# Kernel tuning notes

Measured on AMD Instinct MI355X. Metric: run time of the kernel, lower is better.

## Reference

```python
import jax, jax.numpy as jnp
import numpy as np

NEG_SLOPE = 0.2
EPS = 1e-16


def _gat_conv(x, src, dst, edge_attr, W, We, att_src, att_dst, att_edge, bias):
    """PyG GATConv, heads=H, concat=False, edge_dim given. x:[N,F_in]."""
    N = x.shape[0]
    H, C = att_src.shape
    xs = (x @ W.T).reshape(N, H, C)                      # [N,H,C]
    a_src = jnp.einsum('nhc,hc->nh', xs, att_src)        # [N,H]
    a_dst = jnp.einsum('nhc,hc->nh', xs, att_dst)        # [N,H]
    e = (edge_attr @ We.T).reshape(-1, H, C)             # [E,H,C]
    a_edge = jnp.einsum('ehc,hc->eh', e, att_edge)       # [E,H]
    alpha = a_src[src] + a_dst[dst] + a_edge             # [E,H]
    alpha = jax.nn.leaky_relu(alpha, NEG_SLOPE)
    # segment softmax over destination nodes (per head)
    amax = jax.ops.segment_max(alpha, dst, num_segments=N)   # [N,H]
    ex = jnp.exp(alpha - amax[dst])
    denom = jax.ops.segment_sum(ex, dst, num_segments=N)     # [N,H]
    alpha = ex / (denom[dst] + EPS)
    msg = xs[src] * alpha[..., None]                     # [E,H,C]
    out = jax.ops.segment_sum(msg, dst, num_segments=N)  # [N,H,C]
    return out.mean(axis=1) + bias                       # concat=False -> mean over heads


def _add_self_loops(src, dst, edge_attr, N):
    # PyG add_self_loops with fill_value='mean': per-dst mean of incoming edge_attr
    ones = jnp.ones((edge_attr.shape[0],), edge_attr.dtype)
    sums = jax.ops.segment_sum(edge_attr, dst, num_segments=N)
    cnt = jax.ops.segment_sum(ones, dst, num_segments=N)
    loop_attr = sums / jnp.maximum(cnt, 1.0)[:, None]
    idx = jnp.arange(N, dtype=src.dtype)
    return (jnp.concatenate([src, idx]), jnp.concatenate([dst, idx]),
            jnp.concatenate([edge_attr, loop_attr], axis=0))


def setup_inputs() -> dict:
    key = jax.random.key(0)
    ks = jax.random.split(key, 16)
    N, E, F_IN, C, H = 100000, 1600000, 64, 32, 4
    s = 0.1
    inp = {
        'x': jax.random.normal(ks[0], (N, F_IN), jnp.float32),
        'edge_index': jax.random.randint(ks[1], (2, E), 0, N, jnp.int32),
        'edge_weight': jax.random.uniform(ks[2], (E, 1), jnp.float32),
        'w1': jax.random.normal(ks[3], (H * C, F_IN), jnp.float32) * s,
        'we1': jax.random.normal(ks[4], (H * C, 1), jnp.float32) * s,
        'as1': jax.random.normal(ks[5], (H, C), jnp.float32) * s,
        'ad1': jax.random.normal(ks[6], (H, C), jnp.float32) * s,
        'ae1': jax.random.normal(ks[7], (H, C), jnp.float32) * s,
        'b1': jnp.zeros((C,), jnp.float32),
        'w2': jax.random.normal(ks[8], (H * C, C), jnp.float32) * s,
        'we2': jax.random.normal(ks[9], (H * C, 1), jnp.float32) * s,
        'as2': jax.random.normal(ks[10], (H, C), jnp.float32) * s,
        'ad2': jax.random.normal(ks[11], (H, C), jnp.float32) * s,
        'ae2': jax.random.normal(ks[12], (H, C), jnp.float32) * s,
        'b2': jnp.zeros((C,), jnp.float32),
    }
    return inp


def reference(x, edge_index, edge_weight, w1, we1, as1, ad1, ae1, b1,
              w2, we2, as2, ad2, ae2, b2):
    N = x.shape[0]
    src, dst, ea = _add_self_loops(edge_index[0], edge_index[1], edge_weight, N)
    h = jax.nn.relu(_gat_conv(x, src, dst, ea, w1, we1, as1, ad1, ae1, b1))
    # nn.Dropout is identity in eval mode
    h = jax.nn.relu(_gat_conv(h, src, dst, ea, w2, we2, as2, ad2, ae2, b2))
    return h
```

## Files before the change

### kernel.cpp

```cpp
#include <hip/hip_runtime.h>
#include <hip/hip_fp16.h>
#include <cstddef>

#define GAT_EPS 1e-16f
#define CAP 48

__global__ __launch_bounds__(256, 2)
void k_gemm1h(const float* __restrict__ x, const float* __restrict__ W,
              const float* __restrict__ as_, const float* __restrict__ ad_,
              __half* __restrict__ xs, float* __restrict__ asrc,
              float* __restrict__ adst, int N, int gemmb,
              const int* __restrict__ src, const int* __restrict__ dst,
              const float* __restrict__ ew, int* __restrict__ cnt,
              int2* __restrict__ epk, int E,
              const float* __restrict__ we1, const float* __restrict__ ae1,
              const float* __restrict__ we2, const float* __restrict__ ae2,
              float* __restrict__ wd,
              const float* __restrict__ as2, const float* __restrict__ ad2,
              const float* __restrict__ W2, float* __restrict__ vs2,
              float* __restrict__ vd2) {
    if (blockIdx.x == gridDim.x - 1) {
        int t = threadIdx.x;
        if (t < 128) {
            float v1 = we1[t] * ae1[t];
            float v2 = we2[t] * ae2[t];
#pragma unroll
            for (int off = 16; off; off >>= 1) {
                v1 += __shfl_xor(v1, off);
                v2 += __shfl_xor(v2, off);
            }
            if ((t & 31) == 0) { wd[t >> 5] = v1; wd[4 + (t >> 5)] = v2; }
            int h = t >> 5, c = t & 31;
            float s = 0.f, dv = 0.f;
            for (int k = 0; k < 32; k++) {
                float w = W2[(h * 32 + k) * 32 + c];
                s  += as2[h * 32 + k] * w;
                dv += ad2[h * 32 + k] * w;
            }
            vs2[t] = s;
            vd2[t] = dv;
        }
        return;
    }
    int g = blockIdx.x / 5;
    int r = blockIdx.x % 5;
    if (r != 0) {
        int i = (g * 4 + r - 1) * 256 + threadIdx.x;
        if (i < E) {
            int d = dst[i];
            int p = atomicAdd(&cnt[d], 1);
            p = min(p, CAP - 1);
            int2 q; q.x = src[i]; q.y = __float_as_int(ew[i]);
            epk[(size_t)d * CAP + p] = q;
        }
        return;
    }
    if (g >= gemmb) return;

    int n0 = g * 64;
    int t = threadIdx.x;
    int tx = t & 31;
    int ty = t >> 5;
    __shared__ __half Wh[64 * 132];
    __shared__ float xsh[64 * 65];
    int nrows = min(64, N - n0);
    for (int j = t; j < 8192; j += 256) {
        int c = j >> 6, k = j & 63;
        Wh[k * 132 + ((c & 31) << 2) + (c >> 5)] = __float2half(W[j]);
    }
    const float* xg = x + (size_t)n0 * 64;
    for (int j = t; j < nrows * 64; j += 256) xsh[(j >> 6) * 65 + (j & 63)] = xg[j];
    __syncthreads();

    float acc[8][4];
#pragma unroll
    for (int i = 0; i < 8; i++)
#pragma unroll
        for (int j = 0; j < 4; j++) acc[i][j] = 0.f;

#pragma unroll 4
    for (int k = 0; k < 64; k++) {
        const __half2* wp = reinterpret_cast<const __half2*>(&Wh[k * 132 + (tx << 2)]);
        float2 wf0 = __half22float2(wp[0]);
        float2 wf1 = __half22float2(wp[1]);
#pragma unroll
        for (int i = 0; i < 8; i++) {
            float xv = xsh[(ty * 8 + i) * 65 + k];
            acc[i][0] += xv * wf0.x;
            acc[i][1] += xv * wf0.y;
            acc[i][2] += xv * wf1.x;
            acc[i][3] += xv * wf1.y;
        }
    }

    float asv[4], adv[4];
#pragma unroll
    for (int j = 0; j < 4; j++) { asv[j] = as_[32 * j + tx]; adv[j] = ad_[32 * j + tx]; }

#pragma unroll
    for (int i = 0; i < 8; i++) {
        int row = ty * 8 + i;
        bool ok = row < nrows;
        __half* orow = xs + (size_t)(n0 + row) * 128;
#pragma unroll
        for (int j = 0; j < 4; j++) {
            if (ok) orow[32 * j + tx] = __float2half(acc[i][j]);
            float vs = acc[i][j] * asv[j];
            float vd = acc[i][j] * adv[j];
#pragma unroll
            for (int off = 16; off; off >>= 1) {
                vs += __shfl_xor(vs, off);
                vd += __shfl_xor(vd, off);
            }
            if (ok && tx == 0) {
                asrc[(size_t)(n0 + row) * 4 + j] = vs;
                adst[(size_t)(n0 + row) * 4 + j] = vd;
            }
        }
    }
}

__global__ void k_gather1(const int2* __restrict__ epk, const int* __restrict__ cnt,
                          const __half* __restrict__ xs,
                          const float* __restrict__ asrc, const float* __restrict__ adst,
                          const float* __restrict__ wedot, const float* __restrict__ bias,
                          const float* __restrict__ vs2, const float* __restrict__ vd2,
                          __half2* __restrict__ h1, float* __restrict__ asrc2,
                          float* __restrict__ adst2, int N) {
    int node = blockIdx.x * 4 + (threadIdx.x >> 6);
    if (node >= N) return;
    int l = threadIdx.x & 63;
    int q = l >> 4;
    int p = l & 15;
    int h = p >> 2;
    float wd = wedot[h];
    float ad = adst[(size_t)node * 4 + h];
    int cv = min(cnt[node], CAP);
    int beg = node * CAP;
    int end = beg + cv;

    float a0 = 0.f, a1 = 0.f, a2 = 0.f, a3 = 0.f;
    float a4 = 0.f, a5 = 0.f, a6 = 0.f, a7 = 0.f, ds = 0.f, easum = 0.f;
#pragma unroll 2
    for (int i = beg; i < end; i += 4) {
        int idx = i + q;
        bool valid = idx < end;
        int2 e = epk[valid ? idx : end - 1];
        int s = e.x;
        float eav = valid ? __int_as_float(e.y) : 0.f;
        easum += eav;
        float as = asrc[(size_t)s * 4 + h];
        float al = as + ad + __int_as_float(e.y) * wd;
        al = fmaxf(al, 0.2f * al);
        float w = valid ? __expf(al) : 0.f;
        uint4 raw = reinterpret_cast<const uint4*>(xs + (size_t)s * 128)[p];
        const __half2* hp = reinterpret_cast<const __half2*>(&raw);
        float2 f0 = __half22float2(hp[0]);
        float2 f1 = __half22float2(hp[1]);
        float2 f2 = __half22float2(hp[2]);
        float2 f3 = __half22float2(hp[3]);
        a0 += w * f0.x; a1 += w * f0.y;
        a2 += w * f1.x; a3 += w * f1.y;
        a4 += w * f2.x; a5 += w * f2.y;
        a6 += w * f3.x; a7 += w * f3.y;
        ds += w;
    }
    easum += __shfl_xor(easum, 16);
    easum += __shfl_xor(easum, 32);
    float loop_ea = easum / fmaxf((float)cv, 1.0f);
    float aln = asrc[(size_t)node * 4 + h] + ad + loop_ea * wd;
    aln = fmaxf(aln, 0.2f * aln);
    float wl = __expf(aln);
    if (q == 0) {
        uint4 raw = reinterpret_cast<const uint4*>(xs + (size_t)node * 128)[p];
        const __half2* hp = reinterpret_cast<const __half2*>(&raw);
        float2 f0 = __half22float2(hp[0]);
        float2 f1 = __half22float2(hp[1]);
        float2 f2 = __half22float2(hp[2]);
        float2 f3 = __half22float2(hp[3]);
        a0 += wl * f0.x; a1 += wl * f0.y;
        a2 += wl * f1.x; a3 += wl * f1.y;
        a4 += wl * f2.x; a5 += wl * f2.y;
        a6 += wl * f3.x; a7 += wl * f3.y;
        ds += wl;
    }
    a0 += __shfl_xor(a0, 16); a1 += __shfl_xor(a1, 16);
    a2 += __shfl_xor(a2, 16); a3 += __shfl_xor(a3, 16);
    a4 += __shfl_xor(a4, 16); a5 += __shfl_xor(a5, 16);
    a6 += __shfl_xor(a6, 16); a7 += __shfl_xor(a7, 16);
    ds += __shfl_xor(ds, 16);
    a0 += __shfl_xor(a0, 32); a1 += __shfl_xor(a1, 32);
    a2 += __shfl_xor(a2, 32); a3 += __shfl_xor(a3, 32);
    a4 += __shfl_xor(a4, 32); a5 += __shfl_xor(a5, 32);
    a6 += __shfl_xor(a6, 32); a7 += __shfl_xor(a7, 32);
    ds += __shfl_xor(ds, 32);
    float inv = 1.f / (ds + GAT_EPS);
    a0 *= inv; a1 *= inv; a2 *= inv; a3 *= inv;
    a4 *= inv; a5 *= inv; a6 *= inv; a7 *= inv;
    a0 += __shfl_xor(a0, 4); a1 += __shfl_xor(a1, 4);
    a2 += __shfl_xor(a2, 4); a3 += __shfl_xor(a3, 4);
    a4 += __shfl_xor(a4, 4); a5 += __shfl_xor(a5, 4);
    a6 += __shfl_xor(a6, 4); a7 += __shfl_xor(a7, 4);
    a0 += __shfl_xor(a0, 8); a1 += __shfl_xor(a1, 8);
    a2 += __shfl_xor(a2, 8); a3 += __shfl_xor(a3, 8);
    a4 += __shfl_xor(a4, 8); a5 += __shfl_xor(a5, 8);
    a6 += __shfl_xor(a6, 8); a7 += __shfl_xor(a7, 8);
    if (l < 4) {
        int c0 = l * 8;
        float rv[8];
        rv[0] = fmaxf(0.25f * a0 + bias[c0 + 0], 0.f);
        rv[1] = fmaxf(0.25f * a1 + bias[c0 + 1], 0.f);
        rv[2] = fmaxf(0.25f * a2 + bias[c0 + 2], 0.f);
        rv[3] = fmaxf(0.25f * a3 + bias[c0 + 3], 0.f);
        rv[4] = fmaxf(0.25f * a4 + bias[c0 + 4], 0.f);
        rv[5] = fmaxf(0.25f * a5 + bias[c0 + 5], 0.f);
        rv[6] = fmaxf(0.25f * a6 + bias[c0 + 6], 0.f);
        rv[7] = fmaxf(0.25f * a7 + bias[c0 + 7], 0.f);
        __half2* hp = h1 + (size_t)node * 16 + l * 4;
        hp[0] = __floats2half2_rn(rv[0], rv[1]);
        hp[1] = __floats2half2_rn(rv[2], rv[3]);
        hp[2] = __floats2half2_rn(rv[4], rv[5]);
        hp[3] = __floats2half2_rn(rv[6], rv[7]);
        float pa[4] = {0.f, 0.f, 0.f, 0.f}, pd[4] = {0.f, 0.f, 0.f, 0.f};
#pragma unroll
        for (int hh = 0; hh < 4; hh++)
#pragma unroll
            for (int j = 0; j < 8; j++) {
                pa[hh] += rv[j] * vs2[hh * 32 + c0 + j];
                pd[hh] += rv[j] * vd2[hh * 32 + c0 + j];
            }
#pragma unroll
        for (int hh = 0; hh < 4; hh++) {
            pa[hh] += __shfl_xor(pa[hh], 1);
            pa[hh] += __shfl_xor(pa[hh], 2);
            pd[hh] += __shfl_xor(pd[hh], 1);
            pd[hh] += __shfl_xor(pd[hh], 2);
        }
        if (l == 0) {
            float4 wa, wb;
            wa.x = pa[0]; wa.y = pa[1]; wa.z = pa[2]; wa.w = pa[3];
            wb.x = pd[0]; wb.y = pd[1]; wb.z = pd[2]; wb.w = pd[3];
            *reinterpret_cast<float4*>(asrc2 + (size_t)node * 4) = wa;
            *reinterpret_cast<float4*>(adst2 + (size_t)node * 4) = wb;
        }
    }
}

__global__ void k_gather2(const int2* __restrict__ epk, const int* __restrict__ cnt,
                          const __half2* __restrict__ h1,
                          const float* __restrict__ asrc, const float* __restrict__ adst,
                          const float* __restrict__ wedot, const float* __restrict__ W2,
                          const float* __restrict__ bias, float* __restrict__ out, int N) {
    __shared__ unsigned int Wsh[2180];
    int t = threadIdx.x;
    for (int j = t; j < 2048; j += 256) {
        int rr = j >> 4, kk = j & 15;
        __half2 hv = __floats2half2_rn(W2[rr * 32 + 2 * kk], W2[rr * 32 + 2 * kk + 1]);
        Wsh[rr * 17 + (rr >> 5) + kk] = *reinterpret_cast<unsigned int*>(&hv);
    }
    __syncthreads();
    int node = blockIdx.x * 4 + (t >> 6);
    if (node >= N) return;
    int l = t & 63;
    int q = l >> 4;
    int p = l & 15;
    int h = l & 3;
    int base = l & 48;
    float wd = wedot[h];
    float ad = adst[(size_t)node * 4 + h];
    int cv = min(cnt[node], CAP);
    int beg = node * CAP;
    int end = beg + cv;

    float g00 = 0.f, g01 = 0.f, g10 = 0.f, g11 = 0.f;
    float g20 = 0.f, g21 = 0.f, g30 = 0.f, g31 = 0.f;
    float ds = 0.f, easum = 0.f;
#pragma unroll 2
    for (int i = beg; i < end; i += 4) {
        int idx = i + q;
        bool valid = idx < end;
        int2 e = epk[valid ? idx : end - 1];
        int s = e.x;
        float eav = valid ? __int_as_float(e.y) : 0.f;
        easum += eav;
        float as = asrc[(size_t)s * 4 + h];
        float al = as + ad + __int_as_float(e.y) * wd;
        al = fmaxf(al, 0.2f * al);
        float w = valid ? __expf(al) : 0.f;
        float w0 = __shfl(w, base | 0);
        float w1 = __shfl(w, base | 1);
        float w2v = __shfl(w, base | 2);
        float w3 = __shfl(w, base | 3);
        float2 f = __half22float2(h1[(size_t)s * 16 + p]);
        g00 += w0 * f.x; g01 += w0 * f.y;
        g10 += w1 * f.x; g11 += w1 * f.y;
        g20 += w2v * f.x; g21 += w2v * f.y;
        g30 += w3 * f.x; g31 += w3 * f.y;
        ds += w;
    }
    easum += __shfl_xor(easum, 16);
    easum += __shfl_xor(easum, 32);
    float loop_ea = easum / fmaxf((float)cv, 1.0f);
    float aln = asrc[(size_t)node * 4 + h] + ad + loop_ea * wd;
    aln = fmaxf(aln, 0.2f * aln);
    float wl = __expf(aln);
    float wl0 = __shfl(wl, base | 0);
    float wl1 = __shfl(wl, base | 1);
    float wl2 = __shfl(wl, base | 2);
    float wl3 = __shfl(wl, base | 3);
    if (q == 0) {
        float2 f = __half22float2(h1[(size_t)node * 16 + p]);
        g00 += wl0 * f.x; g01 += wl0 * f.y;
        g10 += wl1 * f.x; g11 += wl1 * f.y;
        g20 += wl2 * f.x; g21 += wl2 * f.y;
        g30 += wl3 * f.x; g31 += wl3 * f.y;
        ds += wl;
    }
    g00 += __shfl_xor(g00, 16); g01 += __shfl_xor(g01, 16);
    g10 += __shfl_xor(g10, 16); g11 += __shfl_xor(g11, 16);
    g20 += __shfl_xor(g20, 16); g21 += __shfl_xor(g21, 16);
    g30 += __shfl_xor(g30, 16); g31 += __shfl_xor(g31, 16);
    g00 += __shfl_xor(g00, 32); g01 += __shfl_xor(g01, 32);
    g10 += __shfl_xor(g10, 32); g11 += __shfl_xor(g11, 32);
    g20 += __shfl_xor(g20, 32); g21 += __shfl_xor(g21, 32);
    g30 += __shfl_xor(g30, 32); g31 += __shfl_xor(g31, 32);
    ds += __shfl_xor(ds, 4);
    ds += __shfl_xor(ds, 8);
    ds += __shfl_xor(ds, 16);
    ds += __shfl_xor(ds, 32);
    float inv_own = 1.f / (0.25f * ds + GAT_EPS);
    float invq = __shfl(inv_own, base | q);
    float gq0, gq1;
    if (q == 0)      { gq0 = g00; gq1 = g01; }
    else if (q == 1) { gq0 = g10; gq1 = g11; }
    else if (q == 2) { gq0 = g20; gq1 = g21; }
    else             { gq0 = g30; gq1 = g31; }
    int rowA17 = ((q << 5) + (p << 1)) * 17 + q;
    float oA = 0.f, oB = 0.f;
#pragma unroll
    for (int kk = 0; kk < 16; kk++) {
        float glo = __shfl(gq0, base | kk);
        float ghi = __shfl(gq1, base | kk);
        unsigned ua = Wsh[rowA17 + kk];
        unsigned ub = Wsh[rowA17 + 17 + kk];
        float2 wa = __half22float2(*reinterpret_cast<__half2*>(&ua));
        float2 wb = __half22float2(*reinterpret_cast<__half2*>(&ub));
        oA += glo * wa.x + ghi * wa.y;
        oB += glo * wb.x + ghi * wb.y;
    }
    oA *= invq; oB *= invq;
    oA += __shfl_xor(oA, 16);
    oA += __shfl_xor(oA, 32);
    oB += __shfl_xor(oB, 16);
    oB += __shfl_xor(oB, 32);
    if (q == 0) {
        float2 r;
        r.x = fmaxf(0.25f * oA + bias[2 * p], 0.f);
        r.y = fmaxf(0.25f * oB + bias[2 * p + 1], 0.f);
        *reinterpret_cast<float2*>(out + (size_t)node * 32 + 2 * p) = r;
    }
}

extern "C" void kernel_launch(void* const* d_in, const int* in_sizes, int n_in,
                              void* d_out, int out_size, void* d_ws, size_t ws_size,
                              hipStream_t stream) {
    const float* x   = (const float*)d_in[0];
    const int*   ei  = (const int*)d_in[1];
    const float* ewt = (const float*)d_in[2];
    const float* w1  = (const float*)d_in[3];
    const float* we1 = (const float*)d_in[4];
    const float* as1 = (const float*)d_in[5];
    const float* ad1 = (const float*)d_in[6];
    const float* ae1 = (const float*)d_in[7];
    const float* b1  = (const float*)d_in[8];
    const float* w2  = (const float*)d_in[9];
    const float* we2 = (const float*)d_in[10];
    const float* as2 = (const float*)d_in[11];
    const float* ad2 = (const float*)d_in[12];
    const float* ae2 = (const float*)d_in[13];
    const float* b2  = (const float*)d_in[14];

    const int N = in_sizes[0] / 64;
    const int E = in_sizes[1] / 2;
    const int* srcI = ei;
    const int* dstI = ei + E;

    char* base = (char*)d_ws;
    size_t off = 0;
    auto alloc = [&](size_t bytes) { char* p = base + off; off += (bytes + 15) & ~(size_t)15; return p; };
    __half* xs     = (__half*)alloc((size_t)N * 128 * sizeof(__half));
    __half2* h1    = (__half2*)alloc((size_t)N * 16 * sizeof(__half2));
    float* asrc    = (float*)alloc((size_t)N * 4 * sizeof(float));
    float* adst    = (float*)alloc((size_t)N * 4 * sizeof(float));
    float* asrc2   = (float*)alloc((size_t)N * 4 * sizeof(float));
    float* adst2   = (float*)alloc((size_t)N * 4 * sizeof(float));
    int*   cnt     = (int*)alloc((size_t)N * sizeof(int));
    int2*  epk     = (int2*)alloc((size_t)N * CAP * sizeof(int2));
    float* wedot   = (float*)alloc(8 * sizeof(float));
    float* vs2     = (float*)alloc(128 * sizeof(float));
    float* vd2     = (float*)alloc(128 * sizeof(float));

    float* outF = (float*)d_out;

    hipMemsetAsync(cnt, 0, (size_t)N * sizeof(int), stream);

    const int gemmb = (N + 63) / 64;
    const int histb = (E + 255) / 256;
    const int G = gemmb > (histb + 3) / 4 ? gemmb : (histb + 3) / 4;
    const int gb = (N + 3) / 4;

    k_gemm1h<<<5 * G + 1, 256, 0, stream>>>(x, w1, as1, ad1, xs, asrc, adst, N, gemmb,
                                            srcI, dstI, ewt, cnt, epk, E,
                                            we1, ae1, we2, ae2, wedot,
                                            as2, ad2, w2, vs2, vd2);

    k_gather1<<<gb, 256, 0, stream>>>(epk, cnt, xs, asrc, adst,
                                      wedot + 0, b1, vs2, vd2, h1, asrc2, adst2, N);

    k_gather2<<<gb, 256, 0, stream>>>(epk, cnt, h1, asrc2, adst2,
                                      wedot + 4, w2, b2, outF, N);
}
```

Baseline: 343.3 us.

## Restructure layer-2 gather with vectorized per-head loads and LDS matvec epilogue

Each lane now owns one head and 8 channels, loading a 16-byte chunk of the source node's fp16 features instead of shuffling per-head weights across lanes. The aggregated per-head vectors are normalized and staged in shared memory. The W2 projection becomes a shared-memory fp32 matvec instead of a shuffle-heavy fp16 loop. This removes many cross-lane shuffles and the fp16 W2 rounding, at the cost of an extra block barrier and more shared memory.

Measured after the change: 321.5 us. 1.07x faster.

```diff
diff --git a/kernel.cpp b/kernel.cpp
--- a/kernel.cpp
+++ b/kernel.cpp
@@ -247,33 +247,35 @@
 }
 
 __global__ void k_gather2(const int2* __restrict__ epk, const int* __restrict__ cnt,
-                          const __half2* __restrict__ h1,
+                          const __half* __restrict__ h1,
                           const float* __restrict__ asrc, const float* __restrict__ adst,
                           const float* __restrict__ wedot, const float* __restrict__ W2,
                           const float* __restrict__ bias, float* __restrict__ out, int N) {
-    __shared__ unsigned int Wsh[2180];
+    __shared__ float W2sh[128 * 33];
+    __shared__ float Ash[4][128];
     int t = threadIdx.x;
-    for (int j = t; j < 2048; j += 256) {
-        int rr = j >> 4, kk = j & 15;
-        __half2 hv = __floats2half2_rn(W2[rr * 32 + 2 * kk], W2[rr * 32 + 2 * kk + 1]);
-        Wsh[rr * 17 + (rr >> 5) + kk] = *reinterpret_cast<unsigned int*>(&hv);
+    for (int j = t; j < 4096; j += 256) {
+        int hh = j >> 10, k = (j >> 5) & 31, c = j & 31;
+        W2sh[(hh * 32 + c) * 33 + k] = W2[j];
     }
     __syncthreads();
-    int node = blockIdx.x * 4 + (t >> 6);
-    if (node >= N) return;
+
+    int node0 = blockIdx.x * 4 + (t >> 6);
+    bool live = node0 < N;
+    int node = live ? node0 : 0;
     int l = t & 63;
     int q = l >> 4;
-    int p = l & 15;
-    int h = l & 3;
-    int base = l & 48;
+    int g = l & 15;
+    int h = g >> 2;
+    int j4 = g & 3;
     float wd = wedot[h];
     float ad = adst[(size_t)node * 4 + h];
     int cv = min(cnt[node], CAP);
     int beg = node * CAP;
     int end = beg + cv;
 
-    float g00 = 0.f, g01 = 0.f, g10 = 0.f, g11 = 0.f;
-    float g20 = 0.f, g21 = 0.f, g30 = 0.f, g31 = 0.f;
+    float A0 = 0.f, A1 = 0.f, A2 = 0.f, A3 = 0.f;
+    float A4 = 0.f, A5 = 0.f, A6 = 0.f, A7 = 0.f;
     float ds = 0.f, easum = 0.f;
 #pragma unroll 2
     for (int i = beg; i < end; i += 4) {
@@ -287,15 +289,16 @@
         float al = as + ad + __int_as_float(e.y) * wd;
         al = fmaxf(al, 0.2f * al);
         float w = valid ? __expf(al) : 0.f;
-        float w0 = __shfl(w, base | 0);
-        float w1 = __shfl(w, base | 1);
-        float w2v = __shfl(w, base | 2);
-        float w3 = __shfl(w, base | 3);
-        float2 f = __half22float2(h1[(size_t)s * 16 + p]);
-        g00 += w0 * f.x; g01 += w0 * f.y;
-        g10 += w1 * f.x; g11 += w1 * f.y;
-        g20 += w2v * f.x; g21 += w2v * f.y;
-        g30 += w3 * f.x; g31 += w3 * f.y;
+        uint4 raw = reinterpret_cast<const uint4*>(h1 + (size_t)s * 32)[j4];
+        const __half2* hp = reinterpret_cast<const __half2*>(&raw);
+        float2 f0 = __half22float2(hp[0]);
+        float2 f1 = __half22float2(hp[1]);
+        float2 f2 = __half22float2(hp[2]);
+        float2 f3 = __half22float2(hp[3]);
+        A0 += w * f0.x; A1 += w * f0.y;
+        A2 += w * f1.x; A3 += w * f1.y;
+        A4 += w * f2.x; A5 += w * f2.y;
+        A6 += w * f3.x; A7 += w * f3.y;
         ds += w;
     }
     easum += __shfl_xor(easum, 16);
@@ -304,61 +307,50 @@
     float aln = asrc[(size_t)node * 4 + h] + ad + loop_ea * wd;
     aln = fmaxf(aln, 0.2f * aln);
     float wl = __expf(aln);
-    float wl0 = __shfl(wl, base | 0);
-    float wl1 = __shfl(wl, base | 1);
-    float wl2 = __shfl(wl, base | 2);
-    float wl3 = __shfl(wl, base | 3);
     if (q == 0) {
-        float2 f = __half22float2(h1[(size_t)node * 16 + p]);
-        g00 += wl0 * f.x; g01 += wl0 * f.y;
-        g10 += wl1 * f.x; g11 += wl1 * f.y;
-        g20 += wl2 * f.x; g21 += wl2 * f.y;
-        g30 += wl3 * f.x; g31 += wl3 * f.y;
+        uint4 raw = reinterpret_cast<const uint4*>(h1 + (size_t)node * 32)[j4];
+        const __half2* hp = reinterpret_cast<const __half2*>(&raw);
+        float2 f0 = __half22float2(hp[0]);
+        float2 f1 = __half22float2(hp[1]);
+        float2 f2 = __half22float2(hp[2]);
+        float2 f3 = __half22float2(hp[3]);
+        A0 += wl * f0.x; A1 += wl * f0.y;
+        A2 += wl * f1.x; A3 += wl * f1.y;
+        A4 += wl * f2.x; A5 += wl * f2.y;
+        A6 += wl * f3.x; A7 += wl * f3.y;
         ds += wl;
     }
-    g00 += __shfl_xor(g00, 16); g01 += __shfl_xor(g01, 16);
-    g10 += __shfl_xor(g10, 16); g11 += __shfl_xor(g11, 16);
-    g20 += __shfl_xor(g20, 16); g21 += __shfl_xor(g21, 16);
-    g30 += __shfl_xor(g30, 16); g31 += __shfl_xor(g31, 16);
-    g00 += __shfl_xor(g00, 32); g01 += __shfl_xor(g01, 32);
-    g10 += __shfl_xor(g10, 32); g11 += __shfl_xor(g11, 32);
-    g20 += __shfl_xor(g20, 32); g21 += __shfl_xor(g21, 32);
-    g30 += __shfl_xor(g30, 32); g31 += __shfl_xor(g31, 32);
-    ds += __shfl_xor(ds, 4);
-    ds += __shfl_xor(ds, 8);
+    A0 += __shfl_xor(A0, 16); A1 += __shfl_xor(A1, 16);
+    A2 += __shfl_xor(A2, 16); A3 += __shfl_xor(A3, 16);
+    A4 += __shfl_xor(A4, 16); A5 += __shfl_xor(A5, 16);
+    A6 += __shfl_xor(A6, 16); A7 += __shfl_xor(A7, 16);
     ds += __shfl_xor(ds, 16);
+    A0 += __shfl_xor(A0, 32); A1 += __shfl_xor(A1, 32);
+    A2 += __shfl_xor(A2, 32); A3 += __shfl_xor(A3, 32);
+    A4 += __shfl_xor(A4, 32); A5 += __shfl_xor(A5, 32);
+    A6 += __shfl_xor(A6, 32); A7 += __shfl_xor(A7, 32);
     ds += __shfl_xor(ds, 32);
-    float inv_own = 1.f / (0.25f * ds + GAT_EPS);
-    float invq = __shfl(inv_own, base | q);
-    float gq0, gq1;
-    if (q == 0)      { gq0 = g00; gq1 = g01; }
-    else if (q == 1) { gq0 = g10; gq1 = g11; }
-    else if (q == 2) { gq0 = g20; gq1 = g21; }
-    else             { gq0 = g30; gq1 = g31; }
-    int rowA17 = ((q << 5) + (p << 1)) * 17 + q;
-    float oA = 0.f, oB = 0.f;
-#pragma unroll
-    for (int kk = 0; kk < 16; kk++) {
-        float glo = __shfl(gq0, base | kk);
-        float ghi = __shfl(gq1, base | kk);
-        unsigned ua = Wsh[rowA17 + kk];
-        unsigned ub = Wsh[rowA17 + 17 + kk];
-        float2 wa = __half22float2(*reinterpret_cast<__half2*>(&ua));
-        float2 wb = __half22float2(*reinterpret_cast<__half2*>(&ub));
-        oA += glo * wa.x + ghi * wa.y;
-        oB += glo * wb.x + ghi * wb.y;
-    }
-    oA *= invq; oB *= invq;
-    oA += __shfl_xor(oA, 16);
-    oA += __shfl_xor(oA, 32);
-    oB += __shfl_xor(oB, 16);
-    oB += __shfl_xor(oB, 32);
+    float inv = 1.f / (ds + GAT_EPS);
     if (q == 0) {
-        float2 r;
-        r.x = fmaxf(0.25f * oA + bias[2 * p], 0.f);
-        r.y = fmaxf(0.25f * oB + bias[2 * p + 1], 0.f);
-        *reinterpret_cast<float2*>(out + (size_t)node * 32 + 2 * p) = r;
-    }
+        float* ap = &Ash[t >> 6][h * 32 + j4 * 8];
+        ap[0] = A0 * inv; ap[1] = A1 * inv; ap[2] = A2 * inv; ap[3] = A3 * inv;
+        ap[4] = A4 * inv; ap[5] = A5 * inv; ap[6] = A6 * inv; ap[7] = A7 * inv;
+    }
+    __syncthreads();
+    int k = l & 31;
+    int hp2 = l >> 5;
+    const float* arow = Ash[t >> 6];
+    float part = 0.f;
+#pragma unroll
+    for (int hh = 2 * hp2; hh <= 2 * hp2 + 1; hh++) {
+        const float* wrow = &W2sh[(hh * 32) * 33 + k];
+#pragma unroll 8
+        for (int c = 0; c < 32; c++)
+            part += arow[hh * 32 + c] * wrow[c * 33];
+    }
+    part += __shfl_xor(part, 32);
+    if (live && l < 32)
+        out[(size_t)node * 32 + k] = fmaxf(0.25f * part + bias[k], 0.f);
 }
 
 extern "C" void kernel_launch(void* const* d_in, const int* in_sizes, int n_in,
@@ -417,6 +409,6 @@
     k_gather1<<<gb, 256, 0, stream>>>(epk, cnt, xs, asrc, adst,
                                       wedot + 0, b1, vs2, vd2, h1, asrc2, adst2, N);
 
-    k_gather2<<<gb, 256, 0, stream>>>(epk, cnt, h1, asrc2, adst2,
+    k_gather2<<<gb, 256, 0, stream>>>(epk, cnt, (const __half*)h1, asrc2, adst2,
                                       wedot + 4, w2, b2, outF, N);
 }
```
